# Kernel tuning notes

Hardware: AMD Instinct MI355X
Metric: run time of the kernel (lower is better)

The kernel has to match this reference:

```python
import jax, jax.numpy as jnp
import numpy as np

MAX_DISP = 4          # init kwarg
WIN = 2 * MAX_DISP + 1  # 9 -> 81 displacement offsets
CHUNK = 16            # hardcoded channel chunk size in the torch module


def setup_inputs() -> dict:
    key = jax.random.key(0)
    k1, k2 = jax.random.split(key)
    B, C, H, W = 8, 128, 96, 160
    x1 = jax.random.normal(k1, (B, C, H, W), dtype=jnp.float32)
    x2 = jax.random.normal(k2, (B, C, H, W), dtype=jnp.float32)
    return {"x1": x1, "x2": x2}


def reference(x1, x2):
    B, C, H, W = x2.shape
    pad = MAX_DISP
    # replicate padding == torch F.pad mode='replicate' == jnp 'edge'
    x2p = jnp.pad(x2, ((0, 0), (0, 0), (pad, pad), (pad, pad)), mode="edge")
    # offsets in the same row-major (dy outer, dx inner) order as the torch loops
    dy, dx = jnp.meshgrid(jnp.arange(-pad, pad + 1), jnp.arange(-pad, pad + 1), indexing="ij")
    offsets = jnp.stack([dy.ravel(), dx.ravel()], axis=1)  # [81, 2]
    num_chunks = -(-C // CHUNK)  # ceil(C/16); with C%16==0 chunk-mean == total-sum/num_chunks

    def body(carry, off):
        # shifted window of x2: x2p[:, :, pad+dy : pad+dy+H, pad+dx : pad+dx+W]
        sl = jax.lax.dynamic_slice(x2p, (0, 0, pad + off[0], pad + off[1]), (B, C, H, W))
        return carry, jnp.sum(x1 * sl, axis=1)  # [B, H, W]

    _, corr = jax.lax.scan(body, None, offsets)  # [81, B, H, W]
    corr = jnp.transpose(corr, (1, 0, 2, 3))     # [B, 81, H, W]
    return corr / jnp.asarray(num_chunks, corr.dtype)
```

## Files before the change

### kernel.cpp

```cpp
#include <hip/hip_runtime.h>
#include <cstdint>

#define BB 8
#define CC 128
#define HH 96
#define WW 160
#define HWsz (HH * WW)
#define TH 8
#define TW 32
#define CSTEP 8
#define HALO_H 16
#define HALO_W 40
#define CH_WORDS (HALO_H * HALO_W)
#define X2_WORDS (CSTEP * CH_WORDS)
#define X1_WORDS (CSTEP * TH * TW)
#define X2_SLOTS (X2_WORDS / 64)
#define X1_SLOTS (X1_WORDS / 64)
#define NWAVES 9
#define NTHREADS (NWAVES * 64)
#define NCHUNKS (CC / CSTEP)
#define NBLOCKS (BB * (HH / TH) * (WW / TW))
#define X1BASE (2 * X2_WORDS)

__device__ __forceinline__ void g2l_dword(const float* g, float* l) {
  __builtin_amdgcn_global_load_lds((const __attribute__((address_space(1))) void*)g,
                                   (__attribute__((address_space(3))) void*)l,
                                   4, 0, 0);
}

extern "C" __global__ void __launch_bounds__(NTHREADS, 2)
corr81_kernel(const float* __restrict__ x1, const float* __restrict__ x2,
              float* __restrict__ out)
{
  __shared__ __align__(16) float lds[2 * X2_WORDS + 2 * X1_WORDS];

  const int tid  = threadIdx.x;
  const int wv   = tid >> 6;
  const int wvu  = __builtin_amdgcn_readfirstlane(wv);
  const int lane = tid & 63;
  const int r    = lane >> 3;
  const int j    = lane & 7;

  const int bid0 = blockIdx.x;
  const int bid  = (bid0 & 7) * (NBLOCKS / 8) + (bid0 >> 3);

  const int wt = bid % (WW / TW);
  const int ht = (bid / (WW / TW)) % (HH / TH);
  const int b  = bid / ((WW / TW) * (HH / TH));
  const int h0 = ht * TH;
  const int w0 = wt * TW;

  uint32_t soff2[9]; uint32_t doff2[9];
#pragma unroll
  for (int i = 0; i < 9; ++i) {
    int idx = wvu + 9 * i; if (idx >= X2_SLOTS) idx = X2_SLOTS - 1;
    const int e   = idx * 64 + lane;
    const int ci  = e / CH_WORDS;
    const int rem = e - ci * CH_WORDS;
    const int hr  = rem / HALO_W;
    const int wh  = rem - hr * HALO_W;
    int gh = h0 + hr - 4; gh = gh < 0 ? 0 : (gh > HH - 1 ? HH - 1 : gh);
    int gw = w0 + wh - 4; gw = gw < 0 ? 0 : (gw > WW - 1 ? WW - 1 : gw);
    soff2[i] = (uint32_t)((ci * HH + gh) * WW + gw);
    doff2[i] = (uint32_t)(idx * 64);
  }
  uint32_t soff1[4]; uint32_t doff1[4];
#pragma unroll
  for (int i = 0; i < 4; ++i) {
    int idx = wvu + 9 * i; if (idx >= X1_SLOTS) idx = X1_SLOTS - 1;
    const int e   = idx * 64 + lane;
    const int ci  = e >> 8;
    const int rem = e & 255;
    const int row = rem >> 5;
    const int col = rem & 31;
    soff1[i] = (uint32_t)(ci * HWsz + (h0 + row) * WW + (w0 + col));
    doff1[i] = (uint32_t)(idx * 64);
  }

  const float* x2b = x2 + (size_t)b * CC * HWsz;
  const float* x1b = x1 + (size_t)b * CC * HWsz;

  float acc[9][4];
#pragma unroll
  for (int d = 0; d < 9; ++d)
#pragma unroll
    for (int p = 0; p < 4; ++p) acc[d][p] = 0.f;

  const int rowbase = (r + wv) * HALO_W + 4 * j;
  const int abase   = r * TW + 4 * j;

#pragma unroll
  for (int i = 0; i < 9; ++i) g2l_dword(x2b + soff2[i], &lds[doff2[i]]);
#pragma unroll
  for (int i = 0; i < 4; ++i) g2l_dword(x1b + soff1[i], &lds[X1BASE + doff1[i]]);

#pragma unroll 1
  for (int k = 0; k < NCHUNKS - 1; ++k) {
    {
      const int nb = (k + 1) & 1;
      const float* s2 = x2b + (size_t)(k + 1) * (CSTEP * HWsz);
      const float* s1 = x1b + (size_t)(k + 1) * (CSTEP * HWsz);
      float* d2 = &lds[nb * X2_WORDS];
      float* d1 = &lds[X1BASE + nb * X1_WORDS];
#pragma unroll
      for (int i = 0; i < 9; ++i) g2l_dword(s2 + soff2[i], d2 + doff2[i]);
#pragma unroll
      for (int i = 0; i < 4; ++i) g2l_dword(s1 + soff1[i], d1 + doff1[i]);
    }

    asm volatile("s_waitcnt vmcnt(13)" ::: "memory");
    __builtin_amdgcn_sched_barrier(0);
    __builtin_amdgcn_s_barrier();
    __builtin_amdgcn_sched_barrier(0);

    {
      const float* xb = &lds[(k & 1) * X2_WORDS] + rowbase;
      const float* ab = &lds[X1BASE + (k & 1) * X1_WORDS] + abase;
#pragma unroll
      for (int ci = 0; ci < CSTEP; ++ci) {
        const float4 a4 = *(const float4*)(ab + ci * (TH * TW));
        const float4* wr = (const float4*)(xb + ci * CH_WORDS);
        const float4 f0 = wr[0];
        const float4 f1 = wr[1];
        const float4 f2 = wr[2];
        const float av[4] = {a4.x, a4.y, a4.z, a4.w};
        const float w12[12] = {f0.x, f0.y, f0.z, f0.w,
                               f1.x, f1.y, f1.z, f1.w,
                               f2.x, f2.y, f2.z, f2.w};
#pragma unroll
        for (int d = 0; d < 9; ++d)
#pragma unroll
          for (int p = 0; p < 4; ++p)
            acc[d][p] = fmaf(av[p], w12[d + p], acc[d][p]);
      }
    }

    __builtin_amdgcn_sched_barrier(0);
    __builtin_amdgcn_s_barrier();
    __builtin_amdgcn_sched_barrier(0);
  }

  asm volatile("s_waitcnt vmcnt(0)" ::: "memory");
  __builtin_amdgcn_sched_barrier(0);
  __builtin_amdgcn_s_barrier();
  __builtin_amdgcn_sched_barrier(0);
  {
    const int k = NCHUNKS - 1;
    const float* xb = &lds[(k & 1) * X2_WORDS] + rowbase;
    const float* ab = &lds[X1BASE + (k & 1) * X1_WORDS] + abase;
#pragma unroll
    for (int ci = 0; ci < CSTEP; ++ci) {
      const float4 a4 = *(const float4*)(ab + ci * (TH * TW));
      const float4* wr = (const float4*)(xb + ci * CH_WORDS);
      const float4 f0 = wr[0];
      const float4 f1 = wr[1];
      const float4 f2 = wr[2];
      const float av[4] = {a4.x, a4.y, a4.z, a4.w};
      const float w12[12] = {f0.x, f0.y, f0.z, f0.w,
                             f1.x, f1.y, f1.z, f1.w,
                             f2.x, f2.y, f2.z, f2.w};
#pragma unroll
      for (int d = 0; d < 9; ++d)
#pragma unroll
        for (int p = 0; p < 4; ++p)
          acc[d][p] = fmaf(av[p], w12[d + p], acc[d][p]);
    }
  }

  float* op = out + (((size_t)b * 81 + (size_t)wv * 9) * HH + (h0 + r)) * WW + (w0 + 4 * j);
#pragma unroll
  for (int d = 0; d < 9; ++d) {
    float4 v;
    v.x = acc[d][0] * 0.125f;
    v.y = acc[d][1] * 0.125f;
    v.z = acc[d][2] * 0.125f;
    v.w = acc[d][3] * 0.125f;
    *(float4*)(op + (size_t)d * HWsz) = v;
  }
}

extern "C" void kernel_launch(void* const* d_in, const int* in_sizes, int n_in,
                              void* d_out, int out_size, void* d_ws, size_t ws_size,
                              hipStream_t stream) {
  const float* x1 = (const float*)d_in[0];
  const float* x2 = (const float*)d_in[1];
  float* out = (float*)d_out;
  corr81_kernel<<<dim3(NBLOCKS), dim3(NTHREADS), 0, stream>>>(x1, x2, out);
}
```

Baseline: 210.2 us.

## Triple-buffer x2 halo tiles and drop the trailing per-chunk barrier

The x2 halo staging in LDS moves from a double buffer to a three-slot ring, so the x2 tile for chunk k+2 is prefetched while chunk k is computed. The x1 prefetch for chunk k+1 is now issued after the compute. Together these remove the second workgroup barrier in each chunk iteration and relax the waitcnt to vmcnt(9). The aim is to cut barrier stalls and give global-to-LDS loads more time to land, at the cost of about 20 KB extra LDS per block, which tightens the two-blocks-per-CU occupancy target.

```diff
diff --git a/kernel.cpp b/kernel.cpp
--- a/kernel.cpp
+++ b/kernel.cpp
@@ -12,15 +12,15 @@
 #define HALO_H 16
 #define HALO_W 40
 #define CH_WORDS (HALO_H * HALO_W)
-#define X2_WORDS (CSTEP * CH_WORDS)
-#define X1_WORDS (CSTEP * TH * TW)
-#define X2_SLOTS (X2_WORDS / 64)
-#define X1_SLOTS (X1_WORDS / 64)
+#define X2W (CSTEP * CH_WORDS)
+#define X1W (CSTEP * TH * TW)
+#define X2_SLOTS (X2W / 64)
+#define X1_SLOTS (X1W / 64)
 #define NWAVES 9
 #define NTHREADS (NWAVES * 64)
 #define NCHUNKS (CC / CSTEP)
 #define NBLOCKS (BB * (HH / TH) * (WW / TW))
-#define X1BASE (2 * X2_WORDS)
+#define X1B (3 * X2W)
 
 __device__ __forceinline__ void g2l_dword(const float* g, float* l) {
   __builtin_amdgcn_global_load_lds((const __attribute__((address_space(1))) void*)g,
@@ -32,7 +32,7 @@
 corr81_kernel(const float* __restrict__ x1, const float* __restrict__ x2,
               float* __restrict__ out)
 {
-  __shared__ __align__(16) float lds[2 * X2_WORDS + 2 * X1_WORDS];
+  __shared__ __align__(16) float lds[3 * X2W + 2 * X1W];
 
   const int tid  = threadIdx.x;
   const int wv   = tid >> 6;
@@ -92,30 +92,26 @@
 #pragma unroll
   for (int i = 0; i < 9; ++i) g2l_dword(x2b + soff2[i], &lds[doff2[i]]);
 #pragma unroll
-  for (int i = 0; i < 4; ++i) g2l_dword(x1b + soff1[i], &lds[X1BASE + doff1[i]]);
+  for (int i = 0; i < 4; ++i) g2l_dword(x1b + soff1[i], &lds[X1B + doff1[i]]);
+  {
+    const float* s2 = x2b + (size_t)(CSTEP * HWsz);
+#pragma unroll
+    for (int i = 0; i < 9; ++i) g2l_dword(s2 + soff2[i], &lds[X2W + doff2[i]]);
+  }
+
+  int rc = 0;
 
 #pragma unroll 1
   for (int k = 0; k < NCHUNKS - 1; ++k) {
-    {
-      const int nb = (k + 1) & 1;
-      const float* s2 = x2b + (size_t)(k + 1) * (CSTEP * HWsz);
-      const float* s1 = x1b + (size_t)(k + 1) * (CSTEP * HWsz);
-      float* d2 = &lds[nb * X2_WORDS];
-      float* d1 = &lds[X1BASE + nb * X1_WORDS];
-#pragma unroll
-      for (int i = 0; i < 9; ++i) g2l_dword(s2 + soff2[i], d2 + doff2[i]);
-#pragma unroll
-      for (int i = 0; i < 4; ++i) g2l_dword(s1 + soff1[i], d1 + doff1[i]);
-    }
-
-    asm volatile("s_waitcnt vmcnt(13)" ::: "memory");
+    __builtin_amdgcn_sched_barrier(0);
+    asm volatile("s_waitcnt vmcnt(9)" ::: "memory");
     __builtin_amdgcn_sched_barrier(0);
     __builtin_amdgcn_s_barrier();
     __builtin_amdgcn_sched_barrier(0);
 
     {
-      const float* xb = &lds[(k & 1) * X2_WORDS] + rowbase;
-      const float* ab = &lds[X1BASE + (k & 1) * X1_WORDS] + abase;
+      const float* xb = &lds[rc] + rowbase;
+      const float* ab = &lds[X1B + (k & 1) * X1W] + abase;
 #pragma unroll
       for (int ci = 0; ci < CSTEP; ++ci) {
         const float4 a4 = *(const float4*)(ab + ci * (TH * TW));
@@ -135,19 +131,32 @@
       }
     }
 
-    __builtin_amdgcn_sched_barrier(0);
-    __builtin_amdgcn_s_barrier();
-    __builtin_amdgcn_sched_barrier(0);
+    {
+      const float* s1 = x1b + (size_t)(k + 1) * (CSTEP * HWsz);
+      float* d1 = &lds[X1B + ((k + 1) & 1) * X1W];
+#pragma unroll
+      for (int i = 0; i < 4; ++i) g2l_dword(s1 + soff1[i], d1 + doff1[i]);
+    }
+    if (k + 2 < NCHUNKS) {
+      int sc = rc + 2 * X2W; if (sc >= 3 * X2W) sc -= 3 * X2W;
+      const float* s2 = x2b + (size_t)(k + 2) * (CSTEP * HWsz);
+      float* d2 = &lds[sc];
+#pragma unroll
+      for (int i = 0; i < 9; ++i) g2l_dword(s2 + soff2[i], d2 + doff2[i]);
+    }
+
+    rc += X2W; if (rc == 3 * X2W) rc = 0;
   }
 
+  __builtin_amdgcn_sched_barrier(0);
   asm volatile("s_waitcnt vmcnt(0)" ::: "memory");
   __builtin_amdgcn_sched_barrier(0);
   __builtin_amdgcn_s_barrier();
   __builtin_amdgcn_sched_barrier(0);
   {
     const int k = NCHUNKS - 1;
-    const float* xb = &lds[(k & 1) * X2_WORDS] + rowbase;
-    const float* ab = &lds[X1BASE + (k & 1) * X1_WORDS] + abase;
+    const float* xb = &lds[rc] + rowbase;
+    const float* ab = &lds[X1B + (k & 1) * X1W] + abase;
 #pragma unroll
     for (int ci = 0; ci < CSTEP; ++ci) {
       const float4 a4 = *(const float4*)(ab + ci * (TH * TW));
```

After: 352.3 us. 67.6% more time.
